# Kernel optimization log

Hardware: AMD Instinct MI355X
Metric: run time of the kernel (lower is better)

## Reference

```python
import jax, jax.numpy as jnp
import numpy as np

OUT_SIZE = 7      # roi_layer out_size
SAMPLE_NUM = 2    # roi_layer sample_num (sampling grid per bin)
STRIDES = (4, 8, 16, 32)


def _roi_align_rotated(feat, rois, spatial_scale):
    """Rotated RoIAlign matching AerialDetection's CUDA kernel.
    feat: [B,C,H,W]; rois: [N,6] = (batch_idx, cx, cy, w, h, theta)."""
    B, C, H, W = feat.shape
    g, P = SAMPLE_NUM, OUT_SIZE
    dt = feat.dtype
    b = rois[:, 0].astype(jnp.int32)
    cx = rois[:, 1] * spatial_scale
    cy = rois[:, 2] * spatial_scale
    rw = rois[:, 3] * spatial_scale
    rh = rois[:, 4] * spatial_scale
    theta = rois[:, 5]
    bin_w = rw / P
    bin_h = rh / P
    pidx = jnp.arange(P, dtype=dt)
    sidx = jnp.arange(g, dtype=dt)
    # local sample offsets relative to roi center, before rotation: [N,P,g]
    off = pidx[None, :, None] + (sidx[None, None, :] + 0.5) / g
    yy = (-rh / 2)[:, None, None] + off * bin_h[:, None, None]
    xx = (-rw / 2)[:, None, None] + off * bin_w[:, None, None]
    yy = yy[:, :, None, :, None]   # [N,P,1,g,1]
    xx = xx[:, None, :, None, :]   # [N,1,P,1,g]
    ct = jnp.cos(theta)[:, None, None, None, None]
    st = jnp.sin(theta)[:, None, None, None, None]
    x = xx * ct + yy * st + cx[:, None, None, None, None]  # [N,P,P,g,g]
    y = yy * ct - xx * st + cy[:, None, None, None, None]
    valid = (y > -1.0) & (y < H) & (x > -1.0) & (x < W)
    y = jnp.maximum(y, 0.0)
    x = jnp.maximum(x, 0.0)
    y0 = jnp.minimum(jnp.floor(y).astype(jnp.int32), H - 1)
    x0 = jnp.minimum(jnp.floor(x).astype(jnp.int32), W - 1)
    y1 = jnp.minimum(y0 + 1, H - 1)
    x1 = jnp.minimum(x0 + 1, W - 1)
    y = jnp.where(y0 >= H - 1, jnp.asarray(H - 1, dt), y)
    x = jnp.where(x0 >= W - 1, jnp.asarray(W - 1, dt), x)
    ly = y - y0
    lx = x - x0
    hy = 1.0 - ly
    hx = 1.0 - lx
    flat = feat.transpose(0, 2, 3, 1).reshape(B * H * W, C)
    b5 = b[:, None, None, None, None]

    def gather(yi, xi):
        return flat[(b5 * H + yi) * W + xi]  # [N,P,P,g,g,C]

    val = (hy * hx)[..., None] * gather(y0, x0) \
        + (hy * lx)[..., None] * gather(y0, x1) \
        + (ly * hx)[..., None] * gather(y1, x0) \
        + (ly * lx)[..., None] * gather(y1, x1)
    val = jnp.where(valid[..., None], val, 0.0)
    out = val.mean(axis=(3, 4))  # average g*g samples -> [N,P,P,C]
    return out.transpose(0, 3, 1, 2)  # [N,C,P,P]


def _conv3x3(x, w, bias):
    y = jax.lax.conv_general_dilated(
        x, w, (1, 1), 'SAME', dimension_numbers=('NCHW', 'OIHW', 'NCHW'))
    return y + bias[None, :, None, None]


def setup_inputs() -> dict:
    key = jax.random.key(0)
    ks = jax.random.split(key, 12)
    B, C, N = 2, 256, 512
    img = 1024.0
    feat0 = jax.random.normal(ks[0], (B, C, 256, 256), jnp.float32)
    feat1 = jax.random.normal(ks[1], (B, C, 128, 128), jnp.float32)
    feat2 = jax.random.normal(ks[2], (B, C, 64, 64), jnp.float32)
    feat3 = jax.random.normal(ks[3], (B, C, 32, 32), jnp.float32)
    b = jax.random.randint(ks[4], (N,), 0, B).astype(jnp.float32)
    cx = jax.random.uniform(ks[5], (N,)) * img
    cy = jax.random.uniform(ks[6], (N,)) * img
    rw = 16.0 + jax.random.uniform(ks[7], (N,)) * 240.0
    rh = 16.0 + jax.random.uniform(ks[8], (N,)) * 240.0
    th = jax.random.uniform(ks[9], (N,)) * np.float32(np.pi)
    rois = jnp.stack([b, cx, cy, rw, rh, th], axis=1)
    pre_w = jax.random.normal(ks[10], (C, C, 3, 3), jnp.float32) * 0.02
    pre_b = jnp.zeros((C,), jnp.float32)
    post_w = jax.random.normal(ks[11], (C, C, 3, 3), jnp.float32) * 0.02
    post_b = jnp.zeros((C,), jnp.float32)
    return {'feat0': feat0, 'feat1': feat1, 'feat2': feat2, 'feat3': feat3,
            'rois': rois, 'pre_w': pre_w, 'pre_b': pre_b,
            'post_w': post_w, 'post_b': post_b}


def reference(feat0, feat1, feat2, feat3, rois, pre_w, pre_b, post_w, post_b):
    acc = 0.0
    for f, s in zip((feat0, feat1, feat2, feat3), STRIDES):
        t = _roi_align_rotated(f, rois, 1.0 / s)
        # pre_conv (ConvModule conv+ReLU); the module's extra ReLU is idempotent
        t = jax.nn.relu(_conv3x3(t, pre_w, pre_b))
        acc = acc + t
    # post_conv (ConvModule conv+ReLU)
    return jax.nn.relu(_conv3x3(acc, post_w, post_b))
```

## Files before the change

kernel.cpp:

```cpp
#include <hip/hip_runtime.h>
#include <hip/hip_bf16.h>

#define P 7
#define CCH 256
#define NPIX 49
#define KTOT 2304
#define THREADS 512
#define TILE 25088
#define ZOFF (2 * TILE)
#define LDSZ (2 * TILE + 512)

typedef __bf16 bf16x8 __attribute__((ext_vector_type(8)));
typedef float f32x4 __attribute__((ext_vector_type(4)));

__device__ __forceinline__ unsigned short f2bf(float f) {
    unsigned int u = __float_as_uint(f);
    unsigned int r = (u + 0x7fffu + ((u >> 16) & 1u)) >> 16;
    return (unsigned short)r;
}
__device__ __forceinline__ float blo(unsigned int u) { return __uint_as_float(u << 16); }
__device__ __forceinline__ float bhi(unsigned int u) { return __uint_as_float(u & 0xffff0000u); }

__global__ void nhwc_transpose_kernel(const float* __restrict__ src,
                                      unsigned short* __restrict__ dst,
                                      int H, int W) {
    __shared__ float tile[32][33];
    int x0 = blockIdx.x * 32;
    int c0 = blockIdx.y * 32;
    int bz = blockIdx.z;
    int b = bz / H, y = bz - b * H;
    int tx = threadIdx.x & 31, ty = threadIdx.x >> 5;
    const float* s = src + ((size_t)(b * CCH + c0) * H + y) * W + x0;
#pragma unroll
    for (int j = 0; j < 4; ++j) {
        int row = ty + j * 8;
        tile[row][tx] = s[(size_t)row * H * W + tx];
    }
    __syncthreads();
    unsigned short* d = dst + ((size_t)bz * W + x0) * CCH + c0;
#pragma unroll
    for (int j = 0; j < 4; ++j) {
        int row = ty + j * 8;
        d[(size_t)row * CCH + tx] = f2bf(tile[tx][row]);
    }
}

__global__ void wtrans_kernel(const float* __restrict__ pre_w,
                              const float* __restrict__ post_w,
                              unsigned short* __restrict__ btpre,
                              unsigned short* __restrict__ btpost) {
    int idx = blockIdx.x * 256 + threadIdx.x;
    const int total = CCH * KTOT;
    if (idx >= 2 * total) return;
    const float* w = pre_w;
    unsigned short* o = btpre;
    int r = idx;
    if (r >= total) { r -= total; w = post_w; o = btpost; }
    int co = r / KTOT, k = r - co * KTOT;
    int t = k >> 8, ci = k & 255;
    o[r] = f2bf(w[(size_t)(co * CCH + ci) * 9 + t]);
}

__launch_bounds__(THREADS, 4)
__global__ void fused_roi_kernel(const float* __restrict__ rois,
                                 const unsigned short* __restrict__ nh0,
                                 const unsigned short* __restrict__ nh1,
                                 const unsigned short* __restrict__ nh2,
                                 const unsigned short* __restrict__ nh3,
                                 const float* __restrict__ raw0,
                                 const float* __restrict__ raw1,
                                 const float* __restrict__ raw2,
                                 const float* __restrict__ raw3,
                                 int modes,
                                 const unsigned short* __restrict__ btpre,
                                 const unsigned short* __restrict__ btpost,
                                 const float* __restrict__ pre_b,
                                 const float* __restrict__ post_b,
                                 float* __restrict__ out) {
    __shared__ __align__(16) char lds[LDSZ];

    int roi  = blockIdx.x;
    int tid  = threadIdx.x;
    int lane = tid & 63;
    int wv   = tid >> 6;
    int lrow = lane & 15;
    int lgrp = lane >> 4;
    int ch0  = lane * 4;
    int co0  = wv * 16 + lrow;
    int co1  = co0 + 128;

    if (tid < 128) ((float*)(lds + ZOFF))[tid] = 0.f;

    const float* rp = rois + (size_t)roi * 6;
    int   bidx = (int)rp[0];
    float cx0 = rp[1], cy0 = rp[2], rw0 = rp[3], rh0 = rp[4], th = rp[5];
    float ct = cosf(th), st = sinf(th);

    const unsigned short* nh[4] = {nh0, nh1, nh2, nh3};
    const float* raw[4] = {raw0, raw1, raw2, raw3};
    const int Hs[4] = {256, 128, 64, 32};
    const float scl[4] = {0.25f, 0.125f, 0.0625f, 0.03125f};

    auto ra_pair = [&](int p) {
        int ml = wv & 1;
        int gl = p * 2 + ml;
        int H = Hs[gl], W = H;
        float s = scl[gl];
        float cx = cx0 * s, cy = cy0 * s, rw = rw0 * s, rh = rh0 * s;
        float bw = rw * (1.0f / P), bh = rh * (1.0f / P);
        float fH = (float)H, fW = (float)W;
        bool staged = (modes >> gl) & 1;
        const unsigned short* f = nh[gl];
        const float* fr = raw[gl];
        for (int bin = (wv >> 1); bin < NPIX; bin += 4) {
            int py = bin / 7, px = bin - py * 7;
            float a0 = 0.f, a1 = 0.f, a2 = 0.f, a3 = 0.f;
#pragma unroll
            for (int smp = 0; smp < 4; ++smp) {
                int sy = smp >> 1, sx = smp & 1;
                float offy = (float)py + 0.25f + 0.5f * (float)sy;
                float offx = (float)px + 0.25f + 0.5f * (float)sx;
                float yy = offy * bh - rh * 0.5f;
                float xx = offx * bw - rw * 0.5f;
                float X = xx * ct + yy * st + cx;
                float Y = yy * ct - xx * st + cy;
                if (Y > -1.0f && Y < fH && X > -1.0f && X < fW) {
                    float Yc = fmaxf(Y, 0.f), Xc = fmaxf(X, 0.f);
                    int y0 = min((int)Yc, H - 1);
                    int x0 = min((int)Xc, W - 1);
                    int y1 = min(y0 + 1, H - 1), x1 = min(x0 + 1, W - 1);
                    if (y0 >= H - 1) Yc = (float)(H - 1);
                    if (x0 >= W - 1) Xc = (float)(W - 1);
                    float ly = Yc - (float)y0, lx = Xc - (float)x0;
                    float hy = 1.f - ly, hx = 1.f - lx;
                    float w00 = hy * hx, w01 = hy * lx, w10 = ly * hx, w11 = ly * lx;
                    if (staged) {
                        size_t r0 = (size_t)(bidx * H + y0) * W;
                        size_t r1 = (size_t)(bidx * H + y1) * W;
                        uint2 u00 = *(const uint2*)(f + ((r0 + x0) << 8) + ch0);
                        uint2 u01 = *(const uint2*)(f + ((r0 + x1) << 8) + ch0);
                        uint2 u10 = *(const uint2*)(f + ((r1 + x0) << 8) + ch0);
                        uint2 u11 = *(const uint2*)(f + ((r1 + x1) << 8) + ch0);
                        a0 += w00 * blo(u00.x) + w01 * blo(u01.x) + w10 * blo(u10.x) + w11 * blo(u11.x);
                        a1 += w00 * bhi(u00.x) + w01 * bhi(u01.x) + w10 * bhi(u10.x) + w11 * bhi(u11.x);
                        a2 += w00 * blo(u00.y) + w01 * blo(u01.y) + w10 * blo(u10.y) + w11 * blo(u11.y);
                        a3 += w00 * bhi(u00.y) + w01 * bhi(u01.y) + w10 * bhi(u10.y) + w11 * bhi(u11.y);
                    } else {
                        size_t hw = (size_t)H * W;
                        size_t i00 = (size_t)y0 * W + x0, i01 = (size_t)y0 * W + x1;
                        size_t i10 = (size_t)y1 * W + x0, i11 = (size_t)y1 * W + x1;
                        const float* fp0 = fr + ((size_t)bidx * CCH + ch0) * hw;
                        float* accp[4] = {&a0, &a1, &a2, &a3};
#pragma unroll
                        for (int cc = 0; cc < 4; ++cc) {
                            const float* fp = fp0 + (size_t)cc * hw;
                            *accp[cc] += w00 * fp[i00] + w01 * fp[i01] + w10 * fp[i10] + w11 * fp[i11];
                        }
                    }
                }
            }
            unsigned int q01 = (unsigned)f2bf(a0 * 0.25f) | ((unsigned)f2bf(a1 * 0.25f) << 16);
            unsigned int q23 = (unsigned)f2bf(a2 * 0.25f) | ((unsigned)f2bf(a3 * 0.25f) << 16);
            int off = ml * TILE + bin * 512 + ((lane * 8) ^ ((bin & 7) << 4));
            *(uint2*)(lds + off) = make_uint2(q01, q23);
        }
    };

    int pys[4], pxs[4];
    bool prow[4];
#pragma unroll
    for (int mt = 0; mt < 4; ++mt) {
        int pix = mt * 16 + lrow;
        pys[mt] = pix / 7;
        pxs[mt] = pix - pys[mt] * 7;
        prow[mt] = pix < NPIX;
    }
    int lg16 = lgrp * 16;

    auto conv_pair = [&](const unsigned short* __restrict__ Bt, f32x4 (&acc)[2][4][2]) {
        const f32x4 FZ = {0.f, 0.f, 0.f, 0.f};
#pragma unroll
        for (int lv = 0; lv < 2; ++lv)
#pragma unroll
            for (int mt = 0; mt < 4; ++mt) {
                acc[lv][mt][0] = FZ; acc[lv][mt][1] = FZ;
            }
        const unsigned short* bp0 = Bt + (size_t)co0 * KTOT + lg16 / 2;
        const unsigned short* bp1 = Bt + (size_t)co1 * KTOT + lg16 / 2;
        for (int t = 0; t < 9; ++t) {
            int dy = t / 3 - 1, dx = (t % 3) - 1;
            int roff[4], swz[4];
#pragma unroll
            for (int mt = 0; mt < 4; ++mt) {
                int oy = pys[mt] + dy, ox = pxs[mt] + dx;
                bool v = prow[mt] && ((unsigned)oy < 7u) && ((unsigned)ox < 7u);
                int np = oy * 7 + ox;
                roff[mt] = v ? np * 512 : ZOFF;
                swz[mt]  = v ? ((np & 7) << 4) : 16;
            }
#pragma unroll
            for (int c8 = 0; c8 < 8; ++c8) {
                int kb = c8 * 64 + lg16;
                int ke = (t * 8 + c8) * 32;
                bf16x8 b0 = *(const bf16x8*)(bp0 + ke);
                bf16x8 b1 = *(const bf16x8*)(bp1 + ke);
#pragma unroll
                for (int mt = 0; mt < 4; ++mt) {
                    int lo = kb ^ swz[mt];
                    bf16x8 a0 = *(const bf16x8*)(lds + roff[mt] + lo);
                    bf16x8 a1 = *(const bf16x8*)(lds + (roff[mt] == ZOFF ? ZOFF : roff[mt] + TILE) + lo);
                    acc[0][mt][0] = __builtin_amdgcn_mfma_f32_16x16x32_bf16(a0, b0, acc[0][mt][0], 0, 0, 0);
                    acc[0][mt][1] = __builtin_amdgcn_mfma_f32_16x16x32_bf16(a0, b1, acc[0][mt][1], 0, 0, 0);
                    acc[1][mt][0] = __builtin_amdgcn_mfma_f32_16x16x32_bf16(a1, b0, acc[1][mt][0], 0, 0, 0);
                    acc[1][mt][1] = __builtin_amdgcn_mfma_f32_16x16x32_bf16(a1, b1, acc[1][mt][1], 0, 0, 0);
                }
            }
        }
    };

    float bs0 = pre_b[co0], bs1 = pre_b[co1];
    f32x4 sum[4][2];
    {
        const f32x4 FZ = {0.f, 0.f, 0.f, 0.f};
#pragma unroll
        for (int mt = 0; mt < 4; ++mt) { sum[mt][0] = FZ; sum[mt][1] = FZ; }
    }

    ra_pair(0);
    __syncthreads();
    {
        f32x4 acc[2][4][2];
        conv_pair(btpre, acc);
#pragma unroll
        for (int lv = 0; lv < 2; ++lv)
#pragma unroll
            for (int mt = 0; mt < 4; ++mt)
#pragma unroll
                for (int r = 0; r < 4; ++r) {
                    sum[mt][0][r] += fmaxf(acc[lv][mt][0][r] + bs0, 0.f);
                    sum[mt][1][r] += fmaxf(acc[lv][mt][1][r] + bs1, 0.f);
                }
    }
    __syncthreads();

    ra_pair(1);
    __syncthreads();
    {
        f32x4 acc[2][4][2];
        conv_pair(btpre, acc);
#pragma unroll
        for (int lv = 0; lv < 2; ++lv)
#pragma unroll
            for (int mt = 0; mt < 4; ++mt)
#pragma unroll
                for (int r = 0; r < 4; ++r) {
                    sum[mt][0][r] += fmaxf(acc[lv][mt][0][r] + bs0, 0.f);
                    sum[mt][1][r] += fmaxf(acc[lv][mt][1][r] + bs1, 0.f);
                }
    }
    __syncthreads();

#pragma unroll
    for (int nt = 0; nt < 2; ++nt) {
        int co = nt ? co1 : co0;
#pragma unroll
        for (int mt = 0; mt < 4; ++mt)
#pragma unroll
            for (int r = 0; r < 4; ++r) {
                int pix = mt * 16 + lgrp * 4 + r;
                if (pix < NPIX) {
                    int off = pix * 512 + ((co * 2) ^ ((pix & 7) << 4));
                    *(unsigned short*)(lds + off) = f2bf(sum[mt][nt][r]);
                }
            }
    }
    __syncthreads();

    f32x4 pacc[4][2];
    {
        const f32x4 FZ = {0.f, 0.f, 0.f, 0.f};
#pragma unroll
        for (int mt = 0; mt < 4; ++mt) { pacc[mt][0] = FZ; pacc[mt][1] = FZ; }
    }
    {
        const unsigned short* bp0 = btpost + (size_t)co0 * KTOT + lg16 / 2;
        const unsigned short* bp1 = btpost + (size_t)co1 * KTOT + lg16 / 2;
        for (int t = 0; t < 9; ++t) {
            int dy = t / 3 - 1, dx = (t % 3) - 1;
            int roff[4], swz[4];
#pragma unroll
            for (int mt = 0; mt < 4; ++mt) {
                int oy = pys[mt] + dy, ox = pxs[mt] + dx;
                bool v = prow[mt] && ((unsigned)oy < 7u) && ((unsigned)ox < 7u);
                int np = oy * 7 + ox;
                roff[mt] = v ? np * 512 : ZOFF;
                swz[mt]  = v ? ((np & 7) << 4) : 16;
            }
#pragma unroll
            for (int c8 = 0; c8 < 8; ++c8) {
                int kb = c8 * 64 + lg16;
                int ke = (t * 8 + c8) * 32;
                bf16x8 b0 = *(const bf16x8*)(bp0 + ke);
                bf16x8 b1 = *(const bf16x8*)(bp1 + ke);
#pragma unroll
                for (int mt = 0; mt < 4; ++mt) {
                    bf16x8 a = *(const bf16x8*)(lds + roff[mt] + (kb ^ swz[mt]));
                    pacc[mt][0] = __builtin_amdgcn_mfma_f32_16x16x32_bf16(a, b0, pacc[mt][0], 0, 0, 0);
                    pacc[mt][1] = __builtin_amdgcn_mfma_f32_16x16x32_bf16(a, b1, pacc[mt][1], 0, 0, 0);
                }
            }
        }
    }

    float pb0 = post_b[co0], pb1 = post_b[co1];
    float* og = out + (size_t)roi * (NPIX * CCH);
#pragma unroll
    for (int mt = 0; mt < 4; ++mt)
#pragma unroll
        for (int r = 0; r < 4; ++r) {
            int pix = mt * 16 + lgrp * 4 + r;
            if (pix < NPIX) {
                og[co0 * NPIX + pix] = fmaxf(pacc[mt][0][r] + pb0, 0.f);
                og[co1 * NPIX + pix] = fmaxf(pacc[mt][1][r] + pb1, 0.f);
            }
        }
}

extern "C" void kernel_launch(void* const* d_in, const int* in_sizes, int n_in,
                              void* d_out, int out_size, void* d_ws, size_t ws_size,
                              hipStream_t stream) {
    const float* feats[4] = {(const float*)d_in[0], (const float*)d_in[1],
                             (const float*)d_in[2], (const float*)d_in[3]};
    const float* rois   = (const float*)d_in[4];
    const float* pre_w  = (const float*)d_in[5];
    const float* pre_b  = (const float*)d_in[6];
    const float* post_w = (const float*)d_in[7];
    const float* post_b = (const float*)d_in[8];

    int nroi = in_sizes[4] / 6;
    int B = in_sizes[0] / (CCH * 256 * 256);
    const int Hs[4] = {256, 128, 64, 32};

    char* ws = (char*)d_ws;
    size_t off = 0;
    auto take = [&](size_t bytes) -> void* {
        void* p = ws + off;
        off += (bytes + 255) & ~(size_t)255;
        return p;
    };
    unsigned short* btpre  = (unsigned short*)take((size_t)CCH * KTOT * 2);
    unsigned short* btpost = (unsigned short*)take((size_t)CCH * KTOT * 2);

    unsigned short* nh[4] = {nullptr, nullptr, nullptr, nullptr};
    int modes = 0;
    for (int l = 0; l < 4; ++l) {
        size_t need = (size_t)B * Hs[l] * Hs[l] * CCH * 2;
        if (off + need <= ws_size) {
            nh[l] = (unsigned short*)take(need);
            modes |= (1 << l);
        }
    }

    for (int l = 0; l < 4; ++l) {
        if (!(modes & (1 << l))) continue;
        dim3 g(Hs[l] / 32, CCH / 32, B * Hs[l]);
        nhwc_transpose_kernel<<<g, 256, 0, stream>>>(feats[l], nh[l], Hs[l], Hs[l]);
    }
    wtrans_kernel<<<(2 * CCH * KTOT + 255) / 256, 256, 0, stream>>>(pre_w, post_w, btpre, btpost);

    fused_roi_kernel<<<nroi, THREADS, 0, stream>>>(rois, nh[0], nh[1], nh[2], nh[3],
                                                   feats[0], feats[1], feats[2], feats[3],
                                                   modes, btpre, btpost, pre_b, post_b,
                                                   (float*)d_out);
}
```

Measured before the change: 381.4 us.

## Split RoI-align staging and conv into separate kernels with a global tile buffer

RoI-align sampling moves into its own kernel that runs one block per (level, roi) and writes swizzled bf16 tiles to a workspace buffer. A second 256-thread conv kernel copies those tiles into LDS and runs both 3x3 convs with MFMA, each wave now covering four output-channel tiles so every A-fragment load feeds more MFMAs. The aim is to stop the sampling phase from stalling tensor-core work, raise parallelism in sampling, and improve operand reuse. The cost is an extra global round trip of the staged tiles, an additional launch, and more accumulator registers per wave. The old fused kernel stays as a fallback when the workspace is too small.

```diff
diff --git a/kernel.cpp b/kernel.cpp
--- a/kernel.cpp
+++ b/kernel.cpp
@@ -5,10 +5,9 @@
 #define CCH 256
 #define NPIX 49
 #define KTOT 2304
-#define THREADS 512
 #define TILE 25088
-#define ZOFF (2 * TILE)
-#define LDSZ (2 * TILE + 512)
+#define ZOFF2 (2 * TILE)
+#define LDS2 (2 * TILE + 512)
 
 typedef __bf16 bf16x8 __attribute__((ext_vector_type(8)));
 typedef float f32x4 __attribute__((ext_vector_type(4)));
@@ -61,7 +60,270 @@
     o[r] = f2bf(w[(size_t)(co * CCH + ci) * 9 + t]);
 }
 
-__launch_bounds__(THREADS, 4)
+__launch_bounds__(256)
+__global__ void ra_stage_kernel(const float* __restrict__ rois,
+                                const unsigned short* __restrict__ nh0,
+                                const unsigned short* __restrict__ nh1,
+                                const unsigned short* __restrict__ nh2,
+                                const unsigned short* __restrict__ nh3,
+                                const float* __restrict__ raw0,
+                                const float* __restrict__ raw1,
+                                const float* __restrict__ raw2,
+                                const float* __restrict__ raw3,
+                                int modes,
+                                unsigned short* __restrict__ atile,
+                                int nroi) {
+    int bid  = blockIdx.x;
+    int lev  = bid / nroi;
+    int roi  = bid - lev * nroi;
+    int tid  = threadIdx.x;
+    int lane = tid & 63;
+    int wv   = tid >> 6;
+    int ch0  = lane * 4;
+
+    const float* rp = rois + (size_t)roi * 6;
+    int   bidx = (int)rp[0];
+    float cx0 = rp[1], cy0 = rp[2], rw0 = rp[3], rh0 = rp[4], th = rp[5];
+    float ct = cosf(th), st = sinf(th);
+
+    const unsigned short* nhv[4] = {nh0, nh1, nh2, nh3};
+    const float* rawv[4] = {raw0, raw1, raw2, raw3};
+    const int Hs[4] = {256, 128, 64, 32};
+    const float scl[4] = {0.25f, 0.125f, 0.0625f, 0.03125f};
+
+    int H = Hs[lev], W = H;
+    float s = scl[lev];
+    float cx = cx0 * s, cy = cy0 * s, rw = rw0 * s, rh = rh0 * s;
+    float bw = rw * (1.0f / P), bh = rh * (1.0f / P);
+    float fH = (float)H, fW = (float)W;
+    bool staged = (modes >> lev) & 1;
+    const unsigned short* f = nhv[lev];
+    const float* fr = rawv[lev];
+
+    char* base = (char*)atile + ((size_t)lev * nroi + roi) * TILE;
+
+    for (int bin = wv; bin < NPIX; bin += 4) {
+        int py = bin / 7, px = bin - py * 7;
+        float a0 = 0.f, a1 = 0.f, a2 = 0.f, a3 = 0.f;
+#pragma unroll
+        for (int smp = 0; smp < 4; ++smp) {
+            int sy = smp >> 1, sx = smp & 1;
+            float offy = (float)py + 0.25f + 0.5f * (float)sy;
+            float offx = (float)px + 0.25f + 0.5f * (float)sx;
+            float yy = offy * bh - rh * 0.5f;
+            float xx = offx * bw - rw * 0.5f;
+            float X = xx * ct + yy * st + cx;
+            float Y = yy * ct - xx * st + cy;
+            if (Y > -1.0f && Y < fH && X > -1.0f && X < fW) {
+                float Yc = fmaxf(Y, 0.f), Xc = fmaxf(X, 0.f);
+                int y0 = min((int)Yc, H - 1);
+                int x0 = min((int)Xc, W - 1);
+                int y1 = min(y0 + 1, H - 1), x1 = min(x0 + 1, W - 1);
+                if (y0 >= H - 1) Yc = (float)(H - 1);
+                if (x0 >= W - 1) Xc = (float)(W - 1);
+                float ly = Yc - (float)y0, lx = Xc - (float)x0;
+                float hy = 1.f - ly, hx = 1.f - lx;
+                float w00 = hy * hx, w01 = hy * lx, w10 = ly * hx, w11 = ly * lx;
+                if (staged) {
+                    size_t r0 = (size_t)(bidx * H + y0) * W;
+                    size_t r1 = (size_t)(bidx * H + y1) * W;
+                    uint2 u00 = *(const uint2*)(f + ((r0 + x0) << 8) + ch0);
+                    uint2 u01 = *(const uint2*)(f + ((r0 + x1) << 8) + ch0);
+                    uint2 u10 = *(const uint2*)(f + ((r1 + x0) << 8) + ch0);
+                    uint2 u11 = *(const uint2*)(f + ((r1 + x1) << 8) + ch0);
+                    a0 += w00 * blo(u00.x) + w01 * blo(u01.x) + w10 * blo(u10.x) + w11 * blo(u11.x);
+                    a1 += w00 * bhi(u00.x) + w01 * bhi(u01.x) + w10 * bhi(u10.x) + w11 * bhi(u11.x);
+                    a2 += w00 * blo(u00.y) + w01 * blo(u01.y) + w10 * blo(u10.y) + w11 * blo(u11.y);
+                    a3 += w00 * bhi(u00.y) + w01 * bhi(u01.y) + w10 * bhi(u10.y) + w11 * bhi(u11.y);
+                } else {
+                    size_t hw = (size_t)H * W;
+                    size_t i00 = (size_t)y0 * W + x0, i01 = (size_t)y0 * W + x1;
+                    size_t i10 = (size_t)y1 * W + x0, i11 = (size_t)y1 * W + x1;
+                    const float* fp0 = fr + ((size_t)bidx * CCH + ch0) * hw;
+                    float* accp[4] = {&a0, &a1, &a2, &a3};
+#pragma unroll
+                    for (int cc = 0; cc < 4; ++cc) {
+                        const float* fp = fp0 + (size_t)cc * hw;
+                        *accp[cc] += w00 * fp[i00] + w01 * fp[i01] + w10 * fp[i10] + w11 * fp[i11];
+                    }
+                }
+            }
+        }
+        unsigned int q01 = (unsigned)f2bf(a0 * 0.25f) | ((unsigned)f2bf(a1 * 0.25f) << 16);
+        unsigned int q23 = (unsigned)f2bf(a2 * 0.25f) | ((unsigned)f2bf(a3 * 0.25f) << 16);
+        int off = bin * 512 + ((lane * 8) ^ ((bin & 7) << 4));
+        *(uint2*)(base + off) = make_uint2(q01, q23);
+    }
+}
+
+__launch_bounds__(256, 2)
+__global__ void conv_all_kernel(const unsigned short* __restrict__ atile,
+                                const unsigned short* __restrict__ btpre,
+                                const unsigned short* __restrict__ btpost,
+                                const float* __restrict__ pre_b,
+                                const float* __restrict__ post_b,
+                                float* __restrict__ out,
+                                int nroi) {
+    __shared__ __align__(16) char lds[LDS2];
+
+    int roi  = blockIdx.x;
+    int tid  = threadIdx.x;
+    int lane = tid & 63;
+    int wv   = tid >> 6;
+    int lrow = lane & 15;
+    int lgrp = lane >> 4;
+
+    if (tid < 128) ((float*)(lds + ZOFF2))[tid] = 0.f;
+
+    int pys[4], pxs[4];
+    bool prow[4];
+#pragma unroll
+    for (int mt = 0; mt < 4; ++mt) {
+        int pix = mt * 16 + lrow;
+        pys[mt] = pix / 7;
+        pxs[mt] = pix - pys[mt] * 7;
+        prow[mt] = pix < NPIX;
+    }
+    int lg16 = lgrp * 16;
+
+    int co[4];
+#pragma unroll
+    for (int nt = 0; nt < 4; ++nt) co[nt] = wv * 16 + lrow + nt * 64;
+
+    auto stage_pair = [&](int p) {
+#pragma unroll
+        for (int ml = 0; ml < 2; ++ml) {
+            const uint4* s = (const uint4*)((const char*)atile +
+                              ((size_t)(p * 2 + ml) * nroi + roi) * TILE);
+            uint4* d = (uint4*)(lds + ml * TILE);
+#pragma unroll
+            for (int it = 0; it < 7; ++it) {
+                int idx = it * 256 + tid;
+                if (idx < TILE / 16) d[idx] = s[idx];
+            }
+        }
+    };
+
+    auto conv_tile = [&](int ml, const unsigned short* __restrict__ Bt,
+                         f32x4 (&acc)[4][4]) {
+        const f32x4 FZ = {0.f, 0.f, 0.f, 0.f};
+#pragma unroll
+        for (int mt = 0; mt < 4; ++mt)
+#pragma unroll
+            for (int nt = 0; nt < 4; ++nt) acc[mt][nt] = FZ;
+        const unsigned short* bp[4];
+#pragma unroll
+        for (int nt = 0; nt < 4; ++nt)
+            bp[nt] = Bt + (size_t)co[nt] * KTOT + lgrp * 8;
+        int tbase = ml * TILE;
+        for (int t = 0; t < 9; ++t) {
+            int dy = t / 3 - 1, dx = (t % 3) - 1;
+            int roff[4], swz[4];
+#pragma unroll
+            for (int mt = 0; mt < 4; ++mt) {
+                int oy = pys[mt] + dy, ox = pxs[mt] + dx;
+                bool v = prow[mt] && ((unsigned)oy < 7u) && ((unsigned)ox < 7u);
+                int np = oy * 7 + ox;
+                roff[mt] = v ? tbase + np * 512 : ZOFF2;
+                swz[mt]  = v ? ((np & 7) << 4) : 16;
+            }
+#pragma unroll
+            for (int c8 = 0; c8 < 8; ++c8) {
+                int kb = c8 * 64 + lg16;
+                int ke = (t * 8 + c8) * 32;
+                bf16x8 b[4];
+#pragma unroll
+                for (int nt = 0; nt < 4; ++nt)
+                    b[nt] = *(const bf16x8*)(bp[nt] + ke);
+#pragma unroll
+                for (int mt = 0; mt < 4; ++mt) {
+                    bf16x8 a = *(const bf16x8*)(lds + roff[mt] + (kb ^ swz[mt]));
+#pragma unroll
+                    for (int nt = 0; nt < 4; ++nt)
+                        acc[mt][nt] = __builtin_amdgcn_mfma_f32_16x16x32_bf16(a, b[nt], acc[mt][nt], 0, 0, 0);
+                }
+            }
+        }
+    };
+
+    float bs[4];
+#pragma unroll
+    for (int nt = 0; nt < 4; ++nt) bs[nt] = pre_b[co[nt]];
+
+    f32x4 sum[4][4];
+    {
+        const f32x4 FZ = {0.f, 0.f, 0.f, 0.f};
+#pragma unroll
+        for (int mt = 0; mt < 4; ++mt)
+#pragma unroll
+            for (int nt = 0; nt < 4; ++nt) sum[mt][nt] = FZ;
+    }
+
+    stage_pair(0);
+    __syncthreads();
+#pragma unroll
+    for (int ml = 0; ml < 2; ++ml) {
+        f32x4 acc[4][4];
+        conv_tile(ml, btpre, acc);
+#pragma unroll
+        for (int mt = 0; mt < 4; ++mt)
+#pragma unroll
+            for (int nt = 0; nt < 4; ++nt)
+#pragma unroll
+                for (int r = 0; r < 4; ++r)
+                    sum[mt][nt][r] += fmaxf(acc[mt][nt][r] + bs[nt], 0.f);
+    }
+    __syncthreads();
+
+    stage_pair(1);
+    __syncthreads();
+#pragma unroll
+    for (int ml = 0; ml < 2; ++ml) {
+        f32x4 acc[4][4];
+        conv_tile(ml, btpre, acc);
+#pragma unroll
+        for (int mt = 0; mt < 4; ++mt)
+#pragma unroll
+            for (int nt = 0; nt < 4; ++nt)
+#pragma unroll
+                for (int r = 0; r < 4; ++r)
+                    sum[mt][nt][r] += fmaxf(acc[mt][nt][r] + bs[nt], 0.f);
+    }
+    __syncthreads();
+
+#pragma unroll
+    for (int nt = 0; nt < 4; ++nt)
+#pragma unroll
+        for (int mt = 0; mt < 4; ++mt)
+#pragma unroll
+            for (int r = 0; r < 4; ++r) {
+                int pix = mt * 16 + lgrp * 4 + r;
+                if (pix < NPIX) {
+                    int off = pix * 512 + ((co[nt] * 2) ^ ((pix & 7) << 4));
+                    *(unsigned short*)(lds + off) = f2bf(sum[mt][nt][r]);
+                }
+            }
+    __syncthreads();
+
+    f32x4 pacc[4][4];
+    conv_tile(0, btpost, pacc);
+
+    float* og = out + (size_t)roi * (NPIX * CCH);
+#pragma unroll
+    for (int nt = 0; nt < 4; ++nt) {
+        float pb = post_b[co[nt]];
+#pragma unroll
+        for (int mt = 0; mt < 4; ++mt)
+#pragma unroll
+            for (int r = 0; r < 4; ++r) {
+                int pix = mt * 16 + lgrp * 4 + r;
+                if (pix < NPIX)
+                    og[co[nt] * NPIX + pix] = fmaxf(pacc[mt][nt][r] + pb, 0.f);
+            }
+    }
+}
+
+__launch_bounds__(512, 4)
 __global__ void fused_roi_kernel(const float* __restrict__ rois,
                                  const unsigned short* __restrict__ nh0,
                                  const unsigned short* __restrict__ nh1,
@@ -77,7 +339,7 @@
                                  const float* __restrict__ pre_b,
                                  const float* __restrict__ post_b,
                                  float* __restrict__ out) {
-    __shared__ __align__(16) char lds[LDSZ];
+    __shared__ __align__(16) char lds[LDS2];
 
     int roi  = blockIdx.x;
     int tid  = threadIdx.x;
@@ -89,7 +351,7 @@
     int co0  = wv * 16 + lrow;
     int co1  = co0 + 128;
 
-    if (tid < 128) ((float*)(lds + ZOFF))[tid] = 0.f;
+    if (tid < 128) ((float*)(lds + ZOFF2))[tid] = 0.f;
 
     const float* rp = rois + (size_t)roi * 6;
     int   bidx = (int)rp[0];
@@ -185,8 +447,8 @@
             for (int mt = 0; mt < 4; ++mt) {
                 acc[lv][mt][0] = FZ; acc[lv][mt][1] = FZ;
             }
-        const unsigned short* bp0 = Bt + (size_t)co0 * KTOT + lg16 / 2;
-        const unsigned short* bp1 = Bt + (size_t)co1 * KTOT + lg16 / 2;
+        const unsigned short* bp0 = Bt + (size_t)co0 * KTOT + lgrp * 8;
+        const unsigned short* bp1 = Bt + (size_t)co1 * KTOT + lgrp * 8;
         for (int t = 0; t < 9; ++t) {
             int dy = t / 3 - 1, dx = (t % 3) - 1;
             int roff[4], swz[4];
@@ -195,7 +457,7 @@
                 int oy = pys[mt] + dy, ox = pxs[mt] + dx;
                 bool v = prow[mt] && ((unsigned)oy < 7u) && ((unsigned)ox < 7u);
                 int np = oy * 7 + ox;
-                roff[mt] = v ? np * 512 : ZOFF;
+                roff[mt] = v ? np * 512 : ZOFF2;
                 swz[mt]  = v ? ((np & 7) << 4) : 16;
             }
 #pragma unroll
@@ -208,7 +470,7 @@
                 for (int mt = 0; mt < 4; ++mt) {
                     int lo = kb ^ swz[mt];
                     bf16x8 a0 = *(const bf16x8*)(lds + roff[mt] + lo);
-                    bf16x8 a1 = *(const bf16x8*)(lds + (roff[mt] == ZOFF ? ZOFF : roff[mt] + TILE) + lo);
+                    bf16x8 a1 = *(const bf16x8*)(lds + (roff[mt] == ZOFF2 ? ZOFF2 : roff[mt] + TILE) + lo);
                     acc[0][mt][0] = __builtin_amdgcn_mfma_f32_16x16x32_bf16(a0, b0, acc[0][mt][0], 0, 0, 0);
                     acc[0][mt][1] = __builtin_amdgcn_mfma_f32_16x16x32_bf16(a0, b1, acc[0][mt][1], 0, 0, 0);
                     acc[1][mt][0] = __builtin_amdgcn_mfma_f32_16x16x32_bf16(a1, b0, acc[1][mt][0], 0, 0, 0);
@@ -283,8 +545,8 @@
         for (int mt = 0; mt < 4; ++mt) { pacc[mt][0] = FZ; pacc[mt][1] = FZ; }
     }
     {
-        const unsigned short* bp0 = btpost + (size_t)co0 * KTOT + lg16 / 2;
-        const unsigned short* bp1 = btpost + (size_t)co1 * KTOT + lg16 / 2;
+        const unsigned short* bp0 = btpost + (size_t)co0 * KTOT + lgrp * 8;
+        const unsigned short* bp1 = btpost + (size_t)co1 * KTOT + lgrp * 8;
         for (int t = 0; t < 9; ++t) {
             int dy = t / 3 - 1, dx = (t % 3) - 1;
             int roff[4], swz[4];
@@ -293,7 +555,7 @@
                 int oy = pys[mt] + dy, ox = pxs[mt] + dx;
                 bool v = prow[mt] && ((unsigned)oy < 7u) && ((unsigned)ox < 7u);
                 int np = oy * 7 + ox;
-                roff[mt] = v ? np * 512 : ZOFF;
+                roff[mt] = v ? np * 512 : ZOFF2;
                 swz[mt]  = v ? ((np & 7) << 4) : 16;
             }
 #pragma unroll
@@ -361,6 +623,11 @@
         }
     }
 
+    size_t abytes = (size_t)4 * nroi * TILE;
+    bool fastpath = (off + ((abytes + 255) & ~(size_t)255)) <= ws_size;
+    unsigned short* atile = nullptr;
+    if (fastpath) atile = (unsigned short*)take(abytes);
+
     for (int l = 0; l < 4; ++l) {
         if (!(modes & (1 << l))) continue;
         dim3 g(Hs[l] / 32, CCH / 32, B * Hs[l]);
@@ -368,8 +635,16 @@
     }
     wtrans_kernel<<<(2 * CCH * KTOT + 255) / 256, 256, 0, stream>>>(pre_w, post_w, btpre, btpost);
 
-    fused_roi_kernel<<<nroi, THREADS, 0, stream>>>(rois, nh[0], nh[1], nh[2], nh[3],
+    if (fastpath) {
+        ra_stage_kernel<<<4 * nroi, 256, 0, stream>>>(rois, nh[0], nh[1], nh[2], nh[3],
+                                                      feats[0], feats[1], feats[2], feats[3],
+                                                      modes, atile, nroi);
+        conv_all_kernel<<<nroi, 256, 0, stream>>>(atile, btpre, btpost, pre_b, post_b,
+                                                  (float*)d_out, nroi);
+    } else {
+        fused_roi_kernel<<<nroi, 512, 0, stream>>>(rois, nh[0], nh[1], nh[2], nh[3],
                                                    feats[0], feats[1], feats[2], feats[3],
                                                    modes, btpre, btpost, pre_b, post_b,
                                                    (float*)d_out);
+    }
 }
```

After: 483.8 us. 1.27x slower.
